# Kernel tuning notes

Hardware: AMD Instinct MI355X
Metric: run time of the kernel (lower is better)

Reference implementation:

```python
import jax, jax.numpy as jnp
import numpy as np

BETA = 0.25

def _l2norm(x, eps=1e-12):
    # F.normalize(x, dim=-1)
    n = jnp.sqrt(jnp.sum(x * x, axis=-1, keepdims=True))
    return x / jnp.maximum(n, eps)

def setup_inputs() -> dict:
    key = jax.random.key(0)
    k1, k2 = jax.random.split(key)
    z = jax.random.normal(k1, (32, 1024, 32), dtype=jnp.float32)
    embedding = jax.random.normal(k2, (8192, 32), dtype=jnp.float32)
    return {"z": z, "embedding": embedding}

def reference(z, embedding):
    B, T, D = z.shape
    zf = _l2norm(z.reshape(-1, D))            # [N, D]
    en = _l2norm(embedding)                   # [n_e, D]
    # squared distances: ||z||^2 + ||e||^2 - 2 z.e  -> [N, n_e]
    d = (jnp.sum(zf * zf, axis=1, keepdims=True)
         + jnp.sum(en * en, axis=1)
         - 2.0 * jnp.einsum('nd,kd->nk', zf, en))
    idx = jnp.argmin(d, axis=1).reshape(B, T)            # [B, T]
    z_q = embedding[idx]                                  # [B, T, D] gather
    z_qnorm = _l2norm(z_q)
    z_norm = _l2norm(z)
    loss = (BETA * jnp.mean((jax.lax.stop_gradient(z_qnorm) - z_norm) ** 2)
            + jnp.mean((z_qnorm - jax.lax.stop_gradient(z_norm)) ** 2))
    # straight-through estimator
    z_q_out = z + jax.lax.stop_gradient(z_qnorm - z)
    return z_q_out, loss, idx
```

## Files before the change

kernel.cpp:

```cpp
#include <hip/hip_runtime.h>
#include <math.h>


#define D 32
#define KCODES 8192
#define MARGIN 2.5e-4f
#define EPS 1e-12f

typedef short bf16x8 __attribute__((ext_vector_type(8)));
typedef unsigned short u16x8 __attribute__((ext_vector_type(8)));
typedef float f32x4 __attribute__((ext_vector_type(4)));

static __device__ __forceinline__ unsigned short f2bf(float x) {
  unsigned u = __float_as_uint(x);
  return (unsigned short)((u + 0x7FFFu + ((u >> 16) & 1u)) >> 16);
}
static __device__ __forceinline__ float bf2f(unsigned short s) {
  return __uint_as_float(((unsigned)s) << 16);
}
static __device__ __forceinline__ void gload_lds16(const void* g, void* l) {
  __builtin_amdgcn_global_load_lds(
      (const __attribute__((address_space(1))) void*)g,
      (__attribute__((address_space(3))) void*)l, 16, 0, 0);
}


__global__ __launch_bounds__(256) void k_prep(const float* __restrict__ z,
                                              const float* __restrict__ emb,
                                              float* __restrict__ en,
                                              float* __restrict__ en_h,
                                              unsigned short* __restrict__ eswz,
                                              unsigned short* __restrict__ zswz_hi,
                                              unsigned short* __restrict__ zswz_lo,
                                              int* __restrict__ cnt,
                                              float* __restrict__ loss,
                                              unsigned long long* __restrict__ mp2,
                                              int N) {
  int v = blockIdx.x * 256 + threadIdx.x;
  if (v == 0) { *cnt = 0; *loss = 0.f; }
  if (v >= KCODES + N) return;
  if (v >= KCODES) mp2[v - KCODES] = 0ull;
  const float* src = (v < KCODES) ? (emb + (size_t)v * D) : (z + (size_t)(v - KCODES) * D);

  float x[D];
  const float4* p = reinterpret_cast<const float4*>(src);
#pragma unroll
  for (int j = 0; j < D / 4; ++j) {
    float4 q = p[j];
    x[4 * j + 0] = q.x; x[4 * j + 1] = q.y; x[4 * j + 2] = q.z; x[4 * j + 3] = q.w;
  }
  float ss = 0.f;
#pragma unroll
  for (int j = 0; j < D; ++j) ss = fmaf(x[j], x[j], ss);
  float n = fmaxf(sqrtf(ss), EPS);
#pragma unroll
  for (int j = 0; j < D; ++j) x[j] = x[j] / n;

  unsigned short hi[D], lo[D];
#pragma unroll
  for (int j = 0; j < D; ++j) {
    hi[j] = f2bf(x[j]);
    lo[j] = f2bf(x[j] - bf2f(hi[j]));
  }

  if (v < KCODES) {
    float4* o = reinterpret_cast<float4*>(en + (size_t)v * D);
    float s2 = 0.f;
#pragma unroll
    for (int j = 0; j < D / 4; ++j) {
      float4 q = {x[4 * j], x[4 * j + 1], x[4 * j + 2], x[4 * j + 3]};
      s2 = fmaf(q.x, q.x, fmaf(q.y, q.y, fmaf(q.z, q.z, fmaf(q.w, q.w, s2))));
      o[j] = q;
    }
    en_h[v] = 0.5f * s2;
    int tl = v >> 4, m = v & 15;
#pragma unroll
    for (int q = 0; q < 4; ++q) {
      u16x8 hv, lv;
#pragma unroll
      for (int j = 0; j < 8; ++j) { hv[j] = hi[8 * q + j]; lv[j] = lo[8 * q + j]; }
      *(u16x8*)(eswz + (size_t)tl * 1024 + (q * 16 + m) * 8) = hv;
      *(u16x8*)(eswz + (size_t)tl * 1024 + 512 + (q * 16 + m) * 8) = lv;
    }
  } else {
    int r = v - KCODES;
    int g = r >> 4, m = r & 15;
#pragma unroll
    for (int q = 0; q < 4; ++q) {
      u16x8 hv, lv;
#pragma unroll
      for (int j = 0; j < 8; ++j) { hv[j] = hi[8 * q + j]; lv[j] = lo[8 * q + j]; }
      *(u16x8*)(zswz_hi + (size_t)g * 512 + (q * 16 + m) * 8) = hv;
      *(u16x8*)(zswz_lo + (size_t)g * 512 + (q * 16 + m) * 8) = lv;
    }
  }
}

__global__ __launch_bounds__(256, 2) void k_argmin_mfma(
    const unsigned short* __restrict__ zswz_hi,
    const unsigned short* __restrict__ zswz_lo,
    const unsigned short* __restrict__ eswz,
    float* __restrict__ res_s1, int* __restrict__ res_cb,
    float* __restrict__ res_s2) {
  __shared__ unsigned short lds_sh[2][16384];

  const int tid = threadIdx.x;
  const int wid = tid >> 6, lane = tid & 63;
  const int lane15 = lane & 15, quad = lane >> 4;
  const int rs = blockIdx.x >> 2;
  const int qt = blockIdx.x & 3;

  bf16x8 zhi[4], zlo[4];
#pragma unroll
  for (int rg = 0; rg < 4; ++rg) {
    int g = rs * 16 + wid * 4 + rg;
    zhi[rg] = *(const bf16x8*)(zswz_hi + (size_t)g * 512 + lane * 8);
    zlo[rg] = *(const bf16x8*)(zswz_lo + (size_t)g * 512 + lane * 8);
  }

  float cm[4], s1g[4], s2c[4];
  int cb[4];
#pragma unroll
  for (int rg = 0; rg < 4; ++rg) {
    cm[rg] = -3.4e38f; s1g[rg] = -3.4e38f; s2c[rg] = -3.4e38f; cb[rg] = 0;
  }
  const f32x4 zero4 = {0.f, 0.f, 0.f, 0.f};

  const float4* gall = reinterpret_cast<const float4*>(eswz) + (size_t)qt * 8 * 2048;
#pragma unroll
  for (int i = 0; i < 8; ++i) {
    int off = i * 256 + tid;
    gload_lds16(gall + off, (char*)&lds_sh[0][0] + (size_t)off * 16);
  }

  for (int c = 0; c < 8; ++c) {
    __syncthreads();
    if (c + 1 < 8) {
      const float4* gn = gall + (size_t)(c + 1) * 2048;
      char* dst = (char*)&lds_sh[(c + 1) & 1][0];
#pragma unroll
      for (int i = 0; i < 8; ++i) {
        int off = i * 256 + tid;
        gload_lds16(gn + off, dst + (size_t)off * 16);
      }
    }
    const unsigned short* buf = &lds_sh[c & 1][0];
#pragma unroll
    for (int t = 0; t < 16; ++t) {
      bf16x8 ahi = *(const bf16x8*)(buf + t * 1024 + lane * 8);
      bf16x8 alo = *(const bf16x8*)(buf + t * 1024 + 512 + lane * 8);
#pragma unroll
      for (int rg = 0; rg < 4; ++rg) {
        f32x4 acc = __builtin_amdgcn_mfma_f32_16x16x32_bf16(ahi, zhi[rg], zero4, 0, 0, 0);
        acc = __builtin_amdgcn_mfma_f32_16x16x32_bf16(ahi, zlo[rg], acc, 0, 0, 0);
        acc = __builtin_amdgcn_mfma_f32_16x16x32_bf16(alo, zhi[rg], acc, 0, 0, 0);
        cm[rg] = fmaxf(cm[rg],
                       fmaxf(fmaxf(acc[0], acc[1]), fmaxf(acc[2], acc[3])));
      }
    }
#pragma unroll
    for (int rg = 0; rg < 4; ++rg) {
      float old1 = s1g[rg];
      s2c[rg] = fmaxf(s2c[rg], fminf(cm[rg], old1));
      bool better = cm[rg] > old1;
      cb[rg] = better ? (qt * 8 + c) : cb[rg];
      s1g[rg] = better ? cm[rg] : old1;
      cm[rg] = -3.4e38f;
    }
  }

#pragma unroll
  for (int m = 16; m <= 32; m <<= 1) {
#pragma unroll
    for (int rg = 0; rg < 4; ++rg) {
      float o1 = __shfl_xor(s1g[rg], m, 64);
      float o2 = __shfl_xor(s2c[rg], m, 64);
      int ob = __shfl_xor(cb[rg], m, 64);
      s2c[rg] = fmaxf(fmaxf(s2c[rg], o2), fminf(s1g[rg], o1));
      bool better = o1 > s1g[rg];
      s1g[rg] = better ? o1 : s1g[rg];
      cb[rg] = better ? ob : cb[rg];
    }
  }
  if (quad == 0) {
#pragma unroll
    for (int rg = 0; rg < 4; ++rg) {
      int row = rs * 256 + wid * 64 + rg * 16 + lane15;
      res_s1[(size_t)row * 4 + qt] = s1g[rg];
      res_cb[(size_t)row * 4 + qt] = cb[rg];
      res_s2[(size_t)row * 4 + qt] = s2c[rg];
    }
  }
}

__global__ __launch_bounds__(256) void k_rescore(
    const float* __restrict__ z, const float* __restrict__ en,
    const float* __restrict__ en_h,
    const float* __restrict__ res_s1, const int* __restrict__ res_cb,
    const float* __restrict__ res_s2,
    int* __restrict__ idx_ws, int* __restrict__ list, int* __restrict__ cnt,
    int N) {
  __shared__ float en_s[256 * 36];
  __shared__ float enh_s[256];
  __shared__ int rows_s[2048];
  __shared__ float s2_s[2048];
  __shared__ int nmatch;

  const int tid = threadIdx.x;
  const int c = blockIdx.x >> 4;
  const int sb = blockIdx.x & 15;
  const int rows_per = N >> 4;
  const int r0 = sb * rows_per;

  if (tid == 0) nmatch = 0;
  const float4* e4 = reinterpret_cast<const float4*>(en) + (size_t)c * 2048;
#pragma unroll
  for (int i = 0; i < 8; ++i) {
    int idx = i * 256 + tid;
    float4 v4 = e4[idx];
    int code = idx >> 3, j = idx & 7;
    *reinterpret_cast<float4*>(&en_s[code * 36 + j * 4]) = v4;
  }
  enh_s[tid] = en_h[c * 256 + tid];
  __syncthreads();

  for (int i = 0; i < rows_per / 256; ++i) {
    int row = r0 + i * 256 + tid;
    float s1b = res_s1[(size_t)row * 4 + 0];
    int cbb = res_cb[(size_t)row * 4 + 0];
    float s2b = res_s2[(size_t)row * 4 + 0];
#pragma unroll
    for (int p = 1; p < 4; ++p) {
      float s1p = res_s1[(size_t)row * 4 + p];
      float s2p = res_s2[(size_t)row * 4 + p];
      int cbp = res_cb[(size_t)row * 4 + p];
      s2b = fmaxf(fmaxf(s2b, s2p), fminf(s1b, s1p));
      bool better = s1p > s1b;
      s1b = better ? s1p : s1b;
      cbb = better ? cbp : cbb;
    }
    if (cbb == c) {
      int pos = atomicAdd(&nmatch, 1);
      rows_s[pos] = row;
      s2_s[pos] = s2b;
    }
  }
  __syncthreads();
  const int nm = nmatch;
  const int lane = tid & 63, wid = tid >> 6;

  for (int ri = wid; ri < nm; ri += 4) {
    int row = __builtin_amdgcn_readfirstlane(rows_s[ri]);
    const float* zr = z + (size_t)row * D;
    float v[D];
    float ss = 0.f;
#pragma unroll
    for (int d = 0; d < D; ++d) v[d] = zr[d];
#pragma unroll
    for (int d = 0; d < D; ++d) ss = fmaf(v[d], v[d], ss);
    float n = fmaxf(sqrtf(ss), EPS);
#pragma unroll
    for (int d = 0; d < D; ++d) v[d] = v[d] / n;

    unsigned long long best = 0ull;
#pragma unroll
    for (int cc = 0; cc < 4; ++cc) {
      int kl = lane + cc * 64;
      float a = -enh_s[kl];
      const float* ep = &en_s[kl * 36];
#pragma unroll
      for (int jj = 0; jj < 8; ++jj) {
        float4 e = *reinterpret_cast<const float4*>(&ep[jj * 4]);
        a = fmaf(v[4 * jj + 0], e.x, a);
        a = fmaf(v[4 * jj + 1], e.y, a);
        a = fmaf(v[4 * jj + 2], e.z, a);
        a = fmaf(v[4 * jj + 3], e.w, a);
      }
      int k = c * 256 + kl;
      unsigned o = __float_as_uint(a);
      o = (o & 0x80000000u) ? ~o : (o | 0x80000000u);
      unsigned long long pk = ((unsigned long long)o << 32) | (unsigned)(8191 - k);
      best = (pk > best) ? pk : best;
    }
#pragma unroll
    for (int m = 32; m >= 1; m >>= 1) {
      unsigned long long op = __shfl_xor(best, m, 64);
      best = (op > best) ? op : best;
    }
    if (lane == 0) {
      unsigned uo = (unsigned)(best >> 32);
      unsigned uu = (uo & 0x80000000u) ? (uo & 0x7FFFFFFFu) : ~uo;
      float sC = __uint_as_float(uu);
      int kC = 8191 - (int)(unsigned)(best & 0xFFFFFFFFull);
      float dotw = sC + enh_s[kC - c * 256];
      if (s2_s[ri] > dotw - MARGIN) {
        int pos = atomicAdd(cnt, 1);
        list[pos] = row;
        idx_ws[row] = -(pos + 1);
      } else {
        idx_ws[row] = kC;
      }
    }
  }
}

__global__ __launch_bounds__(256) void k_cleanup(const float* __restrict__ z,
                                                 const float* __restrict__ en,
                                                 const float* __restrict__ en_h,
                                                 const int* __restrict__ list,
                                                 const int* __restrict__ cnt,
                                                 unsigned long long* __restrict__ mp2) {
  __shared__ unsigned long long wred[4];
  const int tid = threadIdx.x;
  const int lane = tid & 63, wid = tid >> 6;
  const int ntask = (*cnt) * 32;

  for (int j = blockIdx.x; j < ntask; j += gridDim.x) {
    int i = j >> 5, kc = j & 31;
    int row = list[i];
    const float* zr = z + (size_t)row * D;
    float v[D];
    float ss = 0.f;
#pragma unroll
    for (int d = 0; d < D; ++d) v[d] = zr[d];
#pragma unroll
    for (int d = 0; d < D; ++d) ss = fmaf(v[d], v[d], ss);
    float n = fmaxf(sqrtf(ss), EPS);
#pragma unroll
    for (int d = 0; d < D; ++d) v[d] = v[d] / n;

    int k = kc * 256 + tid;
    const float4* er = reinterpret_cast<const float4*>(en + (size_t)k * D);
    float a = -en_h[k];
#pragma unroll
    for (int jj = 0; jj < 8; ++jj) {
      float4 e = er[jj];
      a = fmaf(v[4 * jj + 0], e.x, a);
      a = fmaf(v[4 * jj + 1], e.y, a);
      a = fmaf(v[4 * jj + 2], e.z, a);
      a = fmaf(v[4 * jj + 3], e.w, a);
    }
    unsigned o = __float_as_uint(a);
    o = (o & 0x80000000u) ? ~o : (o | 0x80000000u);
    unsigned long long pk = ((unsigned long long)o << 32) | (unsigned)(8191 - k);
#pragma unroll
    for (int m = 32; m >= 1; m >>= 1) {
      unsigned long long op = __shfl_xor(pk, m, 64);
      pk = (op > pk) ? op : pk;
    }
    if (lane == 0) wred[wid] = pk;
    __syncthreads();
    if (tid == 0) {
      unsigned long long m01 = (wred[0] > wred[1]) ? wred[0] : wred[1];
      unsigned long long m23 = (wred[2] > wred[3]) ? wred[2] : wred[3];
      atomicMax(&mp2[i], (m01 > m23) ? m01 : m23);
    }
    __syncthreads();
  }
}

__global__ __launch_bounds__(256) void k_epi(const float* __restrict__ z,
                                             const float* __restrict__ en,
                                             const int* __restrict__ idx_ws,
                                             const unsigned long long* __restrict__ mp2,
                                             float* __restrict__ out_z,
                                             float* __restrict__ loss,
                                             float* __restrict__ out_idx,
                                             float scale) {
  int row = blockIdx.x * 256 + threadIdx.x;
  int kb = idx_ws[row];
  if (kb < 0) {
    unsigned long long m = mp2[-kb - 1];
    kb = 8191 - (int)(unsigned)(m & 0xFFFFFFFFull);
  }
  out_idx[row] = (float)kb;

  const float4* p = reinterpret_cast<const float4*>(z + (size_t)row * D);
  float4 q[D / 4];
#pragma unroll
  for (int j = 0; j < D / 4; ++j) q[j] = p[j];
  float ss = 0.f;
#pragma unroll
  for (int j = 0; j < D / 4; ++j)
    ss = fmaf(q[j].x, q[j].x, fmaf(q[j].y, q[j].y, fmaf(q[j].z, q[j].z, fmaf(q[j].w, q[j].w, ss))));
  float n = fmaxf(sqrtf(ss), EPS);

  const float4* ep = reinterpret_cast<const float4*>(en + (size_t)kb * D);
  float4* op = reinterpret_cast<float4*>(out_z + (size_t)row * D);
  float s = 0.f;
#pragma unroll
  for (int j = 0; j < D / 4; ++j) {
    float4 e = ep[j];
    float4 o;
    o.x = q[j].x + (e.x - q[j].x);
    o.y = q[j].y + (e.y - q[j].y);
    o.z = q[j].z + (e.z - q[j].z);
    o.w = q[j].w + (e.w - q[j].w);
    op[j] = o;
    float dx = e.x - q[j].x / n;  float dy = e.y - q[j].y / n;
    float dz = e.z - q[j].z / n;  float dw = e.w - q[j].w / n;
    s = fmaf(dx, dx, fmaf(dy, dy, fmaf(dz, dz, fmaf(dw, dw, s))));
  }

#pragma unroll
  for (int off = 32; off > 0; off >>= 1) s += __shfl_down(s, off, 64);
  __shared__ float wsum[4];
  int lane = threadIdx.x & 63, wid = threadIdx.x >> 6;
  if (lane == 0) wsum[wid] = s;
  __syncthreads();
  if (threadIdx.x == 0) {
    float tt = (wsum[0] + wsum[1]) + (wsum[2] + wsum[3]);
    atomicAdd(loss, tt * scale);
  }
}

extern "C" void kernel_launch(void* const* d_in, const int* in_sizes, int n_in,
                              void* d_out, int out_size, void* d_ws, size_t ws_size,
                              hipStream_t stream) {
  const float* z = (const float*)d_in[0];
  const float* emb = (const float*)d_in[1];
  const int N = in_sizes[0] / D;
  const int K = in_sizes[1] / D;

  float* out = (float*)d_out;
  float* out_z = out;
  float* loss = out + (size_t)N * D;
  float* out_idx = out + (size_t)N * D + 1;

  char* w = (char*)d_ws;
  float* en = (float*)w;                         w += (size_t)K * D * 4;
  float* en_h = (float*)w;                       w += (size_t)K * 4;
  unsigned short* eswz = (unsigned short*)w;     w += (size_t)K * D * 2 * 2;
  unsigned short* zswz_hi = (unsigned short*)w;  w += (size_t)N * D * 2;
  unsigned short* zswz_lo = (unsigned short*)w;  w += (size_t)N * D * 2;
  int* idx_ws = (int*)w;                         w += (size_t)N * 4;
  int* list = (int*)w;                           w += (size_t)N * 4;
  unsigned long long* mp2 = (unsigned long long*)w; w += (size_t)N * 8;
  float* res_s1 = (float*)w;                     w += (size_t)N * 4 * 4;
  int* res_cb = (int*)w;                         w += (size_t)N * 4 * 4;
  float* res_s2 = (float*)w;                     w += (size_t)N * 4 * 4;
  int* cnt = (int*)w;

  k_prep<<<dim3((K + N) / 256), 256, 0, stream>>>(
      z, emb, en, en_h, eswz, zswz_hi, zswz_lo, cnt, loss, mp2, N);

  k_argmin_mfma<<<dim3((N / 256) * 4), 256, 0, stream>>>(
      zswz_hi, zswz_lo, eswz, res_s1, res_cb, res_s2);

  k_rescore<<<dim3(32 * 16), 256, 0, stream>>>(
      z, en, en_h, res_s1, res_cb, res_s2, idx_ws, list, cnt, N);

  k_cleanup<<<dim3(4096), 256, 0, stream>>>(z, en, en_h, list, cnt, mp2);

  k_epi<<<dim3(N / 256), 256, 0, stream>>>(
      z, en, idx_ws, mp2, out_z, loss, out_idx, 1.25f / (float)((size_t)N * D));
}
```

Measured before the change: 199.6 us.

## Precompute per-row merge and normalized z to cut redundant rescore work

Adds a k_merge kernel that collapses the four per-quarter argmin partials into one codebook id and second-best score per row, so each of the 512 rescore blocks reads one int per row instead of re-merging twelve values. The prep kernel now also writes the normalized z rows into the output buffer, and rescore and cleanup read them directly instead of recomputing the norm and division. This adds one kernel launch and extra writes in prep. It relies on k_epi overwriting out_z after zn is no longer needed.

```diff
diff --git a/kernel.cpp b/kernel.cpp
--- a/kernel.cpp
+++ b/kernel.cpp
@@ -32,6 +32,7 @@
                                               unsigned short* __restrict__ eswz,
                                               unsigned short* __restrict__ zswz_hi,
                                               unsigned short* __restrict__ zswz_lo,
+                                              float* __restrict__ zn,
                                               int* __restrict__ cnt,
                                               float* __restrict__ loss,
                                               unsigned long long* __restrict__ mp2,
@@ -84,6 +85,12 @@
     }
   } else {
     int r = v - KCODES;
+    float4* zo = reinterpret_cast<float4*>(zn + (size_t)r * D);
+#pragma unroll
+    for (int j = 0; j < D / 4; ++j) {
+      float4 q = {x[4 * j], x[4 * j + 1], x[4 * j + 2], x[4 * j + 3]};
+      zo[j] = q;
+    }
     int g = r >> 4, m = r & 15;
 #pragma unroll
     for (int q = 0; q < 4; ++q) {
@@ -193,17 +200,44 @@
   }
 }
 
+__global__ __launch_bounds__(256) void k_merge(const float* __restrict__ res_s1,
+                                               const int* __restrict__ res_cb,
+                                               const float* __restrict__ res_s2,
+                                               int* __restrict__ row_cb,
+                                               float* __restrict__ row_s2) {
+  int row = blockIdx.x * 256 + threadIdx.x;
+  float4 s1q = reinterpret_cast<const float4*>(res_s1)[row];
+  float4 s2q = reinterpret_cast<const float4*>(res_s2)[row];
+  int4 cbq = reinterpret_cast<const int4*>(res_cb)[row];
+  float s1b = s1q.x;  int cbb = cbq.x;  float s2b = s2q.x;
+  {
+    float s1p = s1q.y, s2p = s2q.y; int cbp = cbq.y;
+    s2b = fmaxf(fmaxf(s2b, s2p), fminf(s1b, s1p));
+    bool better = s1p > s1b;  s1b = better ? s1p : s1b;  cbb = better ? cbp : cbb;
+  }
+  {
+    float s1p = s1q.z, s2p = s2q.z; int cbp = cbq.z;
+    s2b = fmaxf(fmaxf(s2b, s2p), fminf(s1b, s1p));
+    bool better = s1p > s1b;  s1b = better ? s1p : s1b;  cbb = better ? cbp : cbb;
+  }
+  {
+    float s1p = s1q.w, s2p = s2q.w; int cbp = cbq.w;
+    s2b = fmaxf(fmaxf(s2b, s2p), fminf(s1b, s1p));
+    bool better = s1p > s1b;  s1b = better ? s1p : s1b;  cbb = better ? cbp : cbb;
+  }
+  row_cb[row] = cbb;
+  row_s2[row] = s2b;
+}
+
 __global__ __launch_bounds__(256) void k_rescore(
-    const float* __restrict__ z, const float* __restrict__ en,
+    const float* __restrict__ zn, const float* __restrict__ en,
     const float* __restrict__ en_h,
-    const float* __restrict__ res_s1, const int* __restrict__ res_cb,
-    const float* __restrict__ res_s2,
+    const int* __restrict__ row_cb, const float* __restrict__ row_s2,
     int* __restrict__ idx_ws, int* __restrict__ list, int* __restrict__ cnt,
     int N) {
   __shared__ float en_s[256 * 36];
   __shared__ float enh_s[256];
-  __shared__ int rows_s[2048];
-  __shared__ float s2_s[2048];
+  __shared__ unsigned short rows_s[2048];
   __shared__ int nmatch;
 
   const int tid = threadIdx.x;
@@ -225,24 +259,10 @@
   __syncthreads();
 
   for (int i = 0; i < rows_per / 256; ++i) {
-    int row = r0 + i * 256 + tid;
-    float s1b = res_s1[(size_t)row * 4 + 0];
-    int cbb = res_cb[(size_t)row * 4 + 0];
-    float s2b = res_s2[(size_t)row * 4 + 0];
-#pragma unroll
-    for (int p = 1; p < 4; ++p) {
-      float s1p = res_s1[(size_t)row * 4 + p];
-      float s2p = res_s2[(size_t)row * 4 + p];
-      int cbp = res_cb[(size_t)row * 4 + p];
-      s2b = fmaxf(fmaxf(s2b, s2p), fminf(s1b, s1p));
-      bool better = s1p > s1b;
-      s1b = better ? s1p : s1b;
-      cbb = better ? cbp : cbb;
-    }
-    if (cbb == c) {
+    int rrel = i * 256 + tid;
+    if (row_cb[r0 + rrel] == c) {
       int pos = atomicAdd(&nmatch, 1);
-      rows_s[pos] = row;
-      s2_s[pos] = s2b;
+      rows_s[pos] = (unsigned short)rrel;
     }
   }
   __syncthreads();
@@ -250,17 +270,11 @@
   const int lane = tid & 63, wid = tid >> 6;
 
   for (int ri = wid; ri < nm; ri += 4) {
-    int row = __builtin_amdgcn_readfirstlane(rows_s[ri]);
-    const float* zr = z + (size_t)row * D;
+    int row = __builtin_amdgcn_readfirstlane(r0 + (int)rows_s[ri]);
+    const float* znr = zn + (size_t)row * D;
     float v[D];
-    float ss = 0.f;
-#pragma unroll
-    for (int d = 0; d < D; ++d) v[d] = zr[d];
-#pragma unroll
-    for (int d = 0; d < D; ++d) ss = fmaf(v[d], v[d], ss);
-    float n = fmaxf(sqrtf(ss), EPS);
-#pragma unroll
-    for (int d = 0; d < D; ++d) v[d] = v[d] / n;
+#pragma unroll
+    for (int d = 0; d < D; ++d) v[d] = znr[d];
 
     unsigned long long best = 0ull;
 #pragma unroll
@@ -293,7 +307,7 @@
       float sC = __uint_as_float(uu);
       int kC = 8191 - (int)(unsigned)(best & 0xFFFFFFFFull);
       float dotw = sC + enh_s[kC - c * 256];
-      if (s2_s[ri] > dotw - MARGIN) {
+      if (row_s2[row] > dotw - MARGIN) {
         int pos = atomicAdd(cnt, 1);
         list[pos] = row;
         idx_ws[row] = -(pos + 1);
@@ -304,7 +318,7 @@
   }
 }
 
-__global__ __launch_bounds__(256) void k_cleanup(const float* __restrict__ z,
+__global__ __launch_bounds__(256) void k_cleanup(const float* __restrict__ zn,
                                                  const float* __restrict__ en,
                                                  const float* __restrict__ en_h,
                                                  const int* __restrict__ list,
@@ -318,16 +332,10 @@
   for (int j = blockIdx.x; j < ntask; j += gridDim.x) {
     int i = j >> 5, kc = j & 31;
     int row = list[i];
-    const float* zr = z + (size_t)row * D;
+    const float* znr = zn + (size_t)row * D;
     float v[D];
-    float ss = 0.f;
-#pragma unroll
-    for (int d = 0; d < D; ++d) v[d] = zr[d];
-#pragma unroll
-    for (int d = 0; d < D; ++d) ss = fmaf(v[d], v[d], ss);
-    float n = fmaxf(sqrtf(ss), EPS);
-#pragma unroll
-    for (int d = 0; d < D; ++d) v[d] = v[d] / n;
+#pragma unroll
+    for (int d = 0; d < D; ++d) v[d] = znr[d];
 
     int k = kc * 256 + tid;
     const float4* er = reinterpret_cast<const float4*>(en + (size_t)k * D);
@@ -427,6 +435,8 @@
   float* loss = out + (size_t)N * D;
   float* out_idx = out + (size_t)N * D + 1;
 
+  float* zn = out_z;
+
   char* w = (char*)d_ws;
   float* en = (float*)w;                         w += (size_t)K * D * 4;
   float* en_h = (float*)w;                       w += (size_t)K * 4;
@@ -439,18 +449,23 @@
   float* res_s1 = (float*)w;                     w += (size_t)N * 4 * 4;
   int* res_cb = (int*)w;                         w += (size_t)N * 4 * 4;
   float* res_s2 = (float*)w;                     w += (size_t)N * 4 * 4;
+  int* row_cb = (int*)w;                         w += (size_t)N * 4;
+  float* row_s2 = (float*)w;                     w += (size_t)N * 4;
   int* cnt = (int*)w;
 
   k_prep<<<dim3((K + N) / 256), 256, 0, stream>>>(
-      z, emb, en, en_h, eswz, zswz_hi, zswz_lo, cnt, loss, mp2, N);
+      z, emb, en, en_h, eswz, zswz_hi, zswz_lo, zn, cnt, loss, mp2, N);
 
   k_argmin_mfma<<<dim3((N / 256) * 4), 256, 0, stream>>>(
       zswz_hi, zswz_lo, eswz, res_s1, res_cb, res_s2);
 
+  k_merge<<<dim3(N / 256), 256, 0, stream>>>(
+      res_s1, res_cb, res_s2, row_cb, row_s2);
+
   k_rescore<<<dim3(32 * 16), 256, 0, stream>>>(
-      z, en, en_h, res_s1, res_cb, res_s2, idx_ws, list, cnt, N);
-
-  k_cleanup<<<dim3(4096), 256, 0, stream>>>(z, en, en_h, list, cnt, mp2);
+      zn, en, en_h, row_cb, row_s2, idx_ws, list, cnt, N);
+
+  k_cleanup<<<dim3(4096), 256, 0, stream>>>(zn, en, en_h, list, cnt, mp2);
 
   k_epi<<<dim3(N / 256), 256, 0, stream>>>(
       z, en, idx_ws, mp2, out_z, loss, out_idx, 1.25f / (float)((size_t)N * D));
```

Result: faster. 172.8 us (-13.4%).
